# Kernel optimization log

Measured on AMD Instinct MI355X. Metric: run time of the kernel, lower is better.

Reference implementation:

```python
import jax, jax.numpy as jnp
import numpy as np

B, LQ, E, R, H = 4, 64, 512, 32, 768
HOP = 2

def _linear(x, W, b):
    return x @ W + b

def setup_inputs() -> dict:
    key = jax.random.key(0)
    ks = jax.random.split(key, 20)
    s = 0.02
    inp = {
        'question_embedding': jax.random.normal(ks[0], (B, LQ, H), jnp.float32),
        'question_mask': jnp.ones((B, LQ), jnp.float32),
        'entity_embedding': jax.random.normal(ks[1], (B, E, H), jnp.float32),
        'rel_embedding': jax.random.normal(ks[2], (B, E, R, H), jnp.float32),
        'adj': jax.random.randint(ks[3], (B, E, R), 0, E, jnp.int32),
        'node_mask': jax.random.bernoulli(ks[4], 0.95, (B, E)).astype(jnp.float32),
        'adj_mask': jax.random.bernoulli(ks[5], 0.9, (B, E, R)).astype(jnp.float32),
        # params (Linear: y = x @ W + b, W is [in, out])
        'proj_W': jax.random.normal(ks[6], (H, H), jnp.float32) * s,
        'proj_b': jnp.zeros((H,), jnp.float32),
        'rproj_W': jax.random.normal(ks[7], (H, H), jnp.float32) * s,
        'rproj_b': jnp.zeros((H,), jnp.float32),
        'msg_W': jax.random.normal(ks[8], (HOP, 2 * H, H), jnp.float32) * s,
        'msg_b': jnp.zeros((HOP, H), jnp.float32),
        'upd_W': jax.random.normal(ks[9], (HOP, 2 * H, H), jnp.float32) * s,
        'upd_b': jnp.zeros((HOP, H), jnp.float32),
        'relscore_W': jax.random.normal(ks[10], (2 * H, 1), jnp.float32) * s,
        'relscore_b': jnp.zeros((1,), jnp.float32),
        'score_W': jax.random.normal(ks[11], (H, 1), jnp.float32) * s,
        'score_b': jnp.zeros((1,), jnp.float32),
    }
    return inp

def reference(question_embedding, question_mask, entity_embedding, rel_embedding,
              adj, node_mask, adj_mask,
              proj_W, proj_b, rproj_W, rproj_b, msg_W, msg_b, upd_W, upd_b,
              relscore_W, relscore_b, score_W, score_b):
    gelu = lambda x: jax.nn.gelu(x, approximate=False)  # torch nn.GELU default is erf
    dtype = rel_embedding.dtype
    NEG = jnp.finfo(dtype).min

    qe = _linear(question_embedding, proj_W, proj_b)          # [B,LQ,H]
    ee = _linear(entity_embedding, proj_W, proj_b)            # [B,E,H]
    re = _linear(rel_embedding, rproj_W, rproj_b)             # [B,E,R,H]

    qm = question_mask[..., None]
    q = jnp.sum(qe * qm, axis=1) / jnp.sum(qm, axis=1)        # [B,H]

    weight_mask = (1.0 - adj_mask) * NEG                      # [B,E,R]
    q_exp = jnp.broadcast_to(q[:, None, None, :], (B, E, R, H))
    weight_logit = (_linear(jnp.concatenate([re, q_exp], -1), relscore_W, relscore_b)
                    .squeeze(-1) + weight_mask)               # [B,E,R]
    weight = adj_mask * jax.nn.softmax(weight_logit, axis=-1) # [B,E,R]

    adj_flat = adj.reshape(B, E * R)
    for k in range(HOP):
        tail = jnp.take_along_axis(ee, adj_flat[:, :, None], axis=1).reshape(B, E, R, H)
        messages = gelu(_linear(jnp.concatenate([re, tail], -1), msg_W[k], msg_b[k]))
        agg = jnp.einsum('berh,ber->beh', messages, weight)
        ee = gelu(_linear(jnp.concatenate([ee, agg], -1), upd_W[k], upd_b[k]))

    node_neg = (1.0 - node_mask[..., None]) * NEG
    ent_score = (_linear(ee, score_W, score_b) + node_neg).squeeze(-1)  # [B,E]

    # triple_sim (computed under no_grad in torch)
    ee_c = jax.lax.stop_gradient(ee)
    q_c = jax.lax.stop_gradient(q)
    q_source = jnp.einsum('bh,beh->be', q_c, ee_c)            # source node e repeated over R
    q_source = jnp.broadcast_to(q_source[:, :, None], (B, E, R)).reshape(B, E * R)
    tail_final = jnp.take_along_axis(ee_c, adj_flat[:, :, None], axis=1)
    q_target = jnp.einsum('bh,bnh->bn', q_c, tail_final)      # [B,E*R]
    triple_sim = q_source + q_target + jax.lax.stop_gradient(weight_logit).reshape(B, E * R)

    return (ee, ent_score, weight_logit, triple_sim)
```

## Files before the change

### kernel.cpp

```cpp
#include <hip/hip_runtime.h>

#define NEGF (-3.0e38f)

#define BB 4
#define LQQ 64
#define EE_N 512
#define RR 32
#define HH 768

#define WS_QBAR 0
#define WS_Q    3072
#define WS_QD   6144
#define WS_WR1C 6656
#define WS_D0   7424
#define WS_D1   8192
#define WS_C0   8960
#define WS_C1   598784
#define WS_EEA  1188608
#define WS_EEB  2761472
#define WS_EEW  4334336
#define WS_W    5907200
#define WS_AGG  5972736
#define WS_SDOT 7545600
#define WS_CKT0 7547648
#define WS_CKT1 7842560
#define WS_PWT  8137472
#define WS_W0BT 8432384
#define WS_W1BT 8727296
#define WS_U0TT 9022208
#define WS_U0BT 9317120
#define WS_U1TT 9612032
#define WS_U1BT 9906944
#define WS_M0TT 10201856
#define WS_M1TT 10496768
#define WS_RELBF 10791680
#define WS_NEED_BYTES 143830016ull

typedef __attribute__((ext_vector_type(8))) short short8v;
typedef __attribute__((ext_vector_type(4))) short short4v;
typedef __attribute__((ext_vector_type(4))) float f32x4;

#define GLOAD_LDS16(gp, lp) __builtin_amdgcn_global_load_lds( \
    (const __attribute__((address_space(1))) void*)(gp), \
    (__attribute__((address_space(3))) void*)(lp), 16, 0, 0)

__device__ __forceinline__ float gelu_erf(float x) {
    return 0.5f * x * (1.0f + erff(x * 0.70710678118654752f));
}

__device__ __forceinline__ unsigned short f2bf(float f) {
    unsigned int u = __float_as_uint(f);
    unsigned int r = (u + 0x7fffu + ((u >> 16) & 1u)) >> 16;
    return (unsigned short)r;
}

__device__ __forceinline__ float bf2f(unsigned short h) {
    return __uint_as_float(((unsigned int)h) << 16);
}

__global__ void k_qbar(const float* __restrict__ QE, const float* __restrict__ QM,
                       float* __restrict__ qbar) {
    int b = blockIdx.x;
    int tid = threadIdx.x;
    float msum = 0.f;
    for (int l = 0; l < LQQ; ++l) msum += QM[b*LQQ + l];
    for (int h = tid; h < HH; h += 256) {
        float s = 0.f;
        for (int l = 0; l < LQQ; ++l)
            s += QM[b*LQQ + l] * QE[((size_t)(b*LQQ + l))*HH + h];
        qbar[b*HH + h] = s / msum;
    }
}

__global__ void k_small2(const float* __restrict__ RW, const float* __restrict__ RB,
                         const float* __restrict__ RSW, const float* __restrict__ RSB,
                         const float* __restrict__ q, float* __restrict__ wr1c,
                         float* __restrict__ qd) {
    const int wid = threadIdx.x >> 6, lane = threadIdx.x & 63;
    const int blk = blockIdx.x;
    if (blk < 192) {
        int row = blk*4 + wid;
        const float* a = RW + (size_t)row*HH;
        float acc = 0.f;
        #pragma unroll
        for (int p = 0; p < 3; ++p) {
            int i4 = (p*64 + lane) << 2;
            float4 x = *(const float4*)(a + i4);
            float4 w = *(const float4*)(RSW + i4);
            acc += x.x*w.x + x.y*w.y + x.z*w.z + x.w*w.w;
        }
        for (int off = 32; off; off >>= 1) acc += __shfl_xor(acc, off);
        if (lane == 0) wr1c[row] = acc;
    } else {
        float acc = 0.f, acc2 = 0.f;
        const float* src = q + wid*HH;
        #pragma unroll
        for (int p = 0; p < 3; ++p) {
            int i4 = (p*64 + lane) << 2;
            float4 x = *(const float4*)(src + i4);
            float4 w = *(const float4*)(RSW + HH + i4);
            acc += x.x*w.x + x.y*w.y + x.z*w.z + x.w*w.w;
            if (wid == 0) {
                float4 rb = *(const float4*)(RB + i4);
                float4 w0 = *(const float4*)(RSW + i4);
                acc2 += rb.x*w0.x + rb.y*w0.y + rb.z*w0.z + rb.w*w0.w;
            }
        }
        for (int off = 32; off; off >>= 1) { acc += __shfl_xor(acc, off); acc2 += __shfl_xor(acc2, off); }
        if (lane == 0) qd[wid] = acc;
        if (wid == 0 && lane == 0) qd[BB] = acc2 + RSB[0];
    }
}

__global__ void k_dk2(const unsigned short* __restrict__ M0tT,
                      const unsigned short* __restrict__ M1tT,
                      const float* __restrict__ RB, const float* __restrict__ MB,
                      float* __restrict__ d0, float* __restrict__ d1) {
    const int gw = blockIdx.x*4 + (threadIdx.x >> 6);
    const int lane = threadIdx.x & 63;
    const int hop = gw >= HH;
    const int n = hop ? gw - HH : gw;
    const unsigned short* row = (hop ? M1tT : M0tT) + (size_t)n*HH;
    float s = 0.f;
    #pragma unroll
    for (int p = 0; p < 3; ++p) {
        int i4 = (p*64 + lane) << 2;
        const unsigned short* hp = row + i4;
        float4 rv = *(const float4*)(RB + i4);
        s += bf2f(hp[0])*rv.x + bf2f(hp[1])*rv.y + bf2f(hp[2])*rv.z + bf2f(hp[3])*rv.w;
    }
    for (int off = 32; off; off >>= 1) s += __shfl_xor(s, off);
    if (lane == 0) (hop ? d1 : d0)[n] = s + MB[hop*HH + n];
}

__global__ __launch_bounds__(256) void gemm_f32(
    const float* __restrict__ A1, const float* __restrict__ W1,
    const float* __restrict__ bias, float* __restrict__ C,
    int M, int N, int K, int act)
{
    __shared__ float Asm[16][68];
    __shared__ float Bs[16][68];
    const int tid = threadIdx.x;
    const int n0 = blockIdx.x * 64;
    const int m0 = blockIdx.y * 64;
    const int tm = tid >> 4;
    const int tn = tid & 15;
    float acc[4][4] = {};
    for (int kk = 0; kk < K; kk += 16) {
        const int ar = tid >> 2;
        const int ak = (tid & 3) << 2;
        float4 av = make_float4(0.f, 0.f, 0.f, 0.f);
        if (m0 + ar < M) av = *(const float4*)(A1 + (size_t)(m0 + ar)*K + kk + ak);
        const int br = tid >> 4;
        const int bc = (tid & 15) << 2;
        float4 bv = *(const float4*)(W1 + (size_t)(kk + br)*N + n0 + bc);
        __syncthreads();
        Asm[ak+0][ar] = av.x; Asm[ak+1][ar] = av.y;
        Asm[ak+2][ar] = av.z; Asm[ak+3][ar] = av.w;
        *(float4*)&Bs[br][bc] = bv;
        __syncthreads();
        #pragma unroll
        for (int k = 0; k < 16; ++k) {
            float4 a4 = *(const float4*)&Asm[k][tm << 2];
            float4 b4 = *(const float4*)&Bs[k][tn << 2];
            float a[4] = {a4.x, a4.y, a4.z, a4.w};
            float b[4] = {b4.x, b4.y, b4.z, b4.w};
            #pragma unroll
            for (int i = 0; i < 4; ++i)
                #pragma unroll
                for (int j = 0; j < 4; ++j)
                    acc[i][j] = fmaf(a[i], b[j], acc[i][j]);
        }
    }
    float4 bb = make_float4(0.f, 0.f, 0.f, 0.f);
    if (bias) bb = *(const float4*)(bias + n0 + (tn << 2));
    float bbv[4] = {bb.x, bb.y, bb.z, bb.w};
    #pragma unroll
    for (int i = 0; i < 4; ++i) {
        int m = m0 + (tm << 2) + i;
        if (m >= M) break;
        #pragma unroll
        for (int j = 0; j < 4; ++j) {
            float v = acc[i][j] + bbv[j];
            if (act) v = gelu_erf(v);
            C[(size_t)m*N + n0 + (tn << 2) + j] = v;
        }
    }
}

__global__ void k_ckt(const float* __restrict__ Ck, unsigned short* __restrict__ CkT) {
    __shared__ float t[32][33];
    const int k0 = blockIdx.x * 32, n0 = blockIdx.y * 32;
    const int tid = threadIdx.x;
    {
        int r = tid >> 3;
        int c4 = (tid & 7) << 2;
        float4 v = *(const float4*)(Ck + (size_t)(k0 + r)*HH + n0 + c4);
        t[r][c4+0] = v.x; t[r][c4+1] = v.y; t[r][c4+2] = v.z; t[r][c4+3] = v.w;
    }
    __syncthreads();
    {
        int n = tid >> 3;
        int k4 = (tid & 7) << 2;
        unsigned short o[4];
        #pragma unroll
        for (int j = 0; j < 4; ++j) o[j] = f2bf(t[k4+j][n]);
        *(uint2*)(CkT + (size_t)(n0 + n)*HH + k0 + k4) = *(const uint2*)o;
    }
}

struct WPairs { const float* s[9]; unsigned short* d[9]; };
__global__ void k_w2bf(WPairs p) {
    __shared__ float t[32][33];
    const float* __restrict__ Ck = p.s[blockIdx.z];
    unsigned short* __restrict__ CkT = p.d[blockIdx.z];
    const int k0 = blockIdx.x * 32, n0 = blockIdx.y * 32;
    const int tid = threadIdx.x;
    {
        int r = tid >> 3;
        int c4 = (tid & 7) << 2;
        float4 v = *(const float4*)(Ck + (size_t)(k0 + r)*HH + n0 + c4);
        t[r][c4+0] = v.x; t[r][c4+1] = v.y; t[r][c4+2] = v.z; t[r][c4+3] = v.w;
    }
    __syncthreads();
    {
        int n = tid >> 3;
        int k4 = (tid & 7) << 2;
        unsigned short o[4];
        #pragma unroll
        for (int j = 0; j < 4; ++j) o[j] = f2bf(t[k4+j][n]);
        *(uint2*)(CkT + (size_t)(n0 + n)*HH + k0 + k4) = *(const uint2*)o;
    }
}

__global__ __launch_bounds__(256) void k_cvt(
    const float* __restrict__ rel, const float* __restrict__ wr1c,
    const float* __restrict__ qd, const float* __restrict__ am,
    unsigned short* __restrict__ relbf, float* __restrict__ logit) {
    const int wid = threadIdx.x >> 6, lane = threadIdx.x & 63;
    const long row = (long)blockIdx.x*4 + wid;
    const float* a = rel + row*HH;
    unsigned short* o = relbf + row*HH;
    float acc = 0.f;
    #pragma unroll
    for (int p = 0; p < 3; ++p) {
        int i4 = (p*64 + lane) << 2;
        float4 x = *(const float4*)(a + i4);
        float4 wv = *(const float4*)(wr1c + i4);
        acc += x.x*wv.x + x.y*wv.y + x.z*wv.z + x.w*wv.w;
        unsigned short h[4] = {f2bf(x.x), f2bf(x.y), f2bf(x.z), f2bf(x.w)};
        *(uint2*)(o + i4) = *(const uint2*)h;
    }
    for (int off = 32; off; off >>= 1) acc += __shfl_xor(acc, off);
    if (lane == 0) {
        int b = (int)(row >> 14);
        logit[row] = acc + qd[b] + qd[BB] + (1.0f - am[row]) * NEGF;
    }
}

__global__ void k_softmax(const float* __restrict__ logit, const float* __restrict__ am,
                          float* __restrict__ weight) {
    int row = blockIdx.x;
    int lane = threadIdx.x;
    if (lane < 32) {
        float l = logit[row*RR + lane];
        float m = l;
        for (int off = 16; off; off >>= 1) m = fmaxf(m, __shfl_xor(m, off, 32));
        float e = expf(l - m);
        float s = e;
        for (int off = 16; off; off >>= 1) s += __shfl_xor(s, off, 32);
        weight[row*RR + lane] = am[row*RR + lane] * e / s;
    }
}

template<int BM>
__global__ __launch_bounds__(256) void gemm_bf16(
    const float* __restrict__ A1, const unsigned short* __restrict__ W1T,
    const float* __restrict__ A2, const unsigned short* __restrict__ W2T,
    const float* __restrict__ bias, float* __restrict__ C, int act)
{
    constexpr int FM = BM / 32;
    constexpr int AC = BM / 16;
    __shared__ alignas(16) unsigned short As[BM*64];
    __shared__ alignas(16) unsigned short Bs[128*64];
    const int tid = threadIdx.x;
    const int n0 = blockIdx.x * 128;
    const int m0 = blockIdx.y * BM;
    const int w = tid >> 6, lane = tid & 63;
    const int wm = w >> 1, wn = w & 1;
    const int l15 = lane & 15, l4 = lane >> 4;
    const int am_row = tid >> 4;
    const int am_col = (tid & 15) * 4;
    const int bm_row = tid >> 3;
    const int bm_col = (tid & 7) * 8;
    f32x4 acc[FM][4];
    #pragma unroll
    for (int i = 0; i < FM; ++i)
        #pragma unroll
        for (int j = 0; j < 4; ++j) acc[i][j] = (f32x4){0.f,0.f,0.f,0.f};
    const int nPass = (A2 != nullptr) ? 2 : 1;
    for (int pass = 0; pass < nPass; ++pass) {
        const float* __restrict__ A = pass ? A2 : A1;
        const unsigned short* __restrict__ WT = pass ? W2T : W1T;
        for (int k0 = 0; k0 < HH; k0 += 64) {
            float4 av[AC];
            #pragma unroll
            for (int c = 0; c < AC; ++c)
                av[c] = *(const float4*)(A + (size_t)(m0 + c*16 + am_row)*HH + k0 + am_col);
            short8v bv[4];
            #pragma unroll
            for (int i = 0; i < 4; ++i)
                bv[i] = *(const short8v*)(WT + (size_t)(n0 + i*32 + bm_row)*HH + k0 + bm_col);
            __syncthreads();
            #pragma unroll
            for (int c = 0; c < AC; ++c) {
                int r = c*16 + am_row;
                short4v h;
                h[0]=(short)f2bf(av[c].x); h[1]=(short)f2bf(av[c].y);
                h[2]=(short)f2bf(av[c].z); h[3]=(short)f2bf(av[c].w);
                int ba = r*128 + ((am_col*2) ^ ((r & 7) << 4));
                *(short4v*)&As[ba >> 1] = h;
            }
            #pragma unroll
            for (int i = 0; i < 4; ++i) {
                int r = i*32 + bm_row;
                int ba = r*128 + ((bm_col*2) ^ ((r & 7) << 4));
                *(short8v*)&Bs[ba >> 1] = bv[i];
            }
            __syncthreads();
            #pragma unroll
            for (int ks = 0; ks < 2; ++ks) {
                const int kb = ks*64 + l4*16;
                short8v af[FM], bf[4];
                #pragma unroll
                for (int fm = 0; fm < FM; ++fm) {
                    int row = wm*(FM*16) + fm*16 + l15;
                    af[fm] = *(const short8v*)&As[(row*128 + (kb ^ ((row & 7) << 4))) >> 1];
                }
                #pragma unroll
                for (int fn = 0; fn < 4; ++fn) {
                    int row = wn*64 + fn*16 + l15;
                    bf[fn] = *(const short8v*)&Bs[(row*128 + (kb ^ ((row & 7) << 4))) >> 1];
                }
                #pragma unroll
                for (int fm = 0; fm < FM; ++fm)
                    #pragma unroll
                    for (int fn = 0; fn < 4; ++fn)
                        acc[fm][fn] = __builtin_amdgcn_mfma_f32_16x16x32_bf16(af[fm], bf[fn], acc[fm][fn], 0, 0, 0);
            }
            __syncthreads();
        }
    }
    #pragma unroll
    for (int fn = 0; fn < 4; ++fn) {
        int col = n0 + wn*64 + fn*16 + l15;
        float bb = bias ? bias[col] : 0.f;
        #pragma unroll
        for (int fm = 0; fm < FM; ++fm) {
            int row0 = m0 + wm*(FM*16) + fm*16 + l4*4;
            #pragma unroll
            for (int j = 0; j < 4; ++j) {
                float v = acc[fm][fn][j] + bb;
                if (act) v = gelu_erf(v);
                C[(size_t)(row0 + j)*HH + col] = v;
            }
        }
    }
}

__global__ __launch_bounds__(256, 3) void k_msg8(
    const unsigned short* __restrict__ relbf, const unsigned short* __restrict__ CkT,
    const float* __restrict__ dk, const float* __restrict__ eeW,
    const float* __restrict__ weight, const int* __restrict__ adj,
    float* __restrict__ agg)
{
    __shared__ alignas(16) unsigned short As[128*64];
    __shared__ alignas(16) unsigned short Bs[128*64];
    int*   adjS = (int*)As;
    float* wS   = (float*)(As + 256);
    const int tid = threadIdx.x;
    const int bid = blockIdx.x;
    const int L = (bid & 7) * 384 + (bid >> 3);
    const int mt = L / 6, nt = L - mt*6;
    const int n0 = nt * 128;
    const int m0 = mt * 128;
    const int be0 = mt * 4;
    const int b = be0 >> 9;
    const int w = tid >> 6, lane = tid & 63;
    const int wm = w >> 1, wn = w & 1;
    const int l15 = lane & 15, l4 = lane >> 4;
    const int crow = lane >> 3;
    const int csl  = (lane & 7) ^ crow;

    f32x4 acc[4][4];
    #pragma unroll
    for (int i = 0; i < 4; ++i)
        #pragma unroll
        for (int j = 0; j < 4; ++j) acc[i][j] = (f32x4){0.f,0.f,0.f,0.f};

    for (int t = 0; t < 12; ++t) {
        const int k0 = t*64;
        #pragma unroll
        for (int c = 0; c < 4; ++c) {
            int rbase = w*32 + c*8;
            GLOAD_LDS16(relbf + (size_t)(m0 + rbase + crow)*HH + k0 + csl*8,
                        &As[rbase*64]);
            GLOAD_LDS16(CkT   + (size_t)(n0 + rbase + crow)*HH + k0 + csl*8,
                        &Bs[rbase*64]);
        }
        __syncthreads();
        #pragma unroll
        for (int ks = 0; ks < 2; ++ks) {
            const int ko = ks*32 + l4*8;
            short8v af[4], bf[4];
            #pragma unroll
            for (int fm = 0; fm < 4; ++fm) {
                int row = wm*64 + fm*16 + l15;
                af[fm] = *(const short8v*)&As[row*64 + (ko ^ ((row & 7) << 3))];
            }
            #pragma unroll
            for (int fn = 0; fn < 4; ++fn) {
                int row = wn*64 + fn*16 + l15;
                bf[fn] = *(const short8v*)&Bs[row*64 + (ko ^ ((row & 7) << 3))];
            }
            #pragma unroll
            for (int fm = 0; fm < 4; ++fm)
                #pragma unroll
                for (int fn = 0; fn < 4; ++fn)
                    acc[fm][fn] = __builtin_amdgcn_mfma_f32_16x16x32_bf16(af[fm], bf[fn], acc[fm][fn], 0, 0, 0);
        }
        __syncthreads();
    }

    if (tid < 128) {
        adjS[tid] = adj[be0*RR + tid];
        wS[tid]   = weight[be0*RR + tid];
    }
    __syncthreads();

    #pragma unroll
    for (int eh = 0; eh < 2; ++eh) {
        const int el = wm*2 + eh;
        const int be = be0 + el;
        #pragma unroll
        for (int fn = 0; fn < 4; ++fn) {
            int col = n0 + wn*64 + fn*16 + l15;
            float d = dk[col];
            float s = 0.f;
            #pragma unroll
            for (int fp = 0; fp < 2; ++fp) {
                const int fm = eh*2 + fp;
                #pragma unroll
                for (int j = 0; j < 4; ++j) {
                    int rr = fp*16 + l4*4 + j;
                    int tl = adjS[el*RR + rr];
                    float tail = eeW[((size_t)(b*EE_N + tl))*HH + col];
                    s += wS[el*RR + rr] * gelu_erf(acc[fm][fn][j] + tail + d);
                }
            }
            s += __shfl_xor(s, 16);
            s += __shfl_xor(s, 32);
            if (l4 == 0) agg[(size_t)be*HH + col] = s;
        }
    }
}

template<int FUSE>
__global__ __launch_bounds__(256, 3) void k_msg6(
    const float* __restrict__ rel, const unsigned short* __restrict__ CkT,
    const float* __restrict__ dk, const float* __restrict__ eeW,
    const float* __restrict__ weight_in, const int* __restrict__ adj,
    const float* __restrict__ wr1c, const float* __restrict__ qd,
    const float* __restrict__ am,
    float* __restrict__ agg, float* __restrict__ logit_out,
    float* __restrict__ weight_out)
{
    __shared__ alignas(16) unsigned short As[64*64];
    __shared__ alignas(16) unsigned short Bs[256*64];
    int*   adjS = (int*)As;
    float* wS   = (float*)(As + 128);
    float* lgS  = (float*)(As + 256);
    const int tid = threadIdx.x;
    const int bid = blockIdx.x;
    const int L = (bid & 7) * 384 + (bid >> 3);
    const int mt = L / 3, nt = L - mt*3;
    const int n0 = nt * 256;
    const int m0 = mt * 64;
    const int be0 = mt * 2;
    const int b = be0 >> 9;
    const int wn = tid >> 6, lane = tid & 63;
    const int l15 = lane & 15, l4 = lane >> 4;
    const int am_row = tid >> 4;
    const int am_col = (tid & 15) * 4;
    const int bm_row = tid >> 3;
    const int bm_col = (tid & 7) * 8;
    const float* apA = rel + (size_t)(m0 + am_row)*HH + am_col;
    const unsigned short* apB = CkT + (size_t)(n0 + bm_row)*HH + bm_col;
    f32x4 acc[4][4];
    #pragma unroll
    for (int i = 0; i < 4; ++i)
        #pragma unroll
        for (int j = 0; j < 4; ++j) acc[i][j] = (f32x4){0.f,0.f,0.f,0.f};
    float lg[4] = {0.f, 0.f, 0.f, 0.f};
    float4 av[4];
    short8v bv[8];
    #pragma unroll
    for (int c = 0; c < 4; ++c) av[c] = *(const float4*)(apA + (size_t)c*16*HH);
    #pragma unroll
    for (int i = 0; i < 8; ++i) bv[i] = *(const short8v*)(apB + (size_t)i*32*HH);
    for (int t = 0; t < 12; ++t) {
        const int k0 = t*64;
        #pragma unroll
        for (int c = 0; c < 4; ++c) {
            int r = c*16 + am_row;
            short4v h;
            h[0]=(short)f2bf(av[c].x); h[1]=(short)f2bf(av[c].y);
            h[2]=(short)f2bf(av[c].z); h[3]=(short)f2bf(av[c].w);
            int ba = r*128 + ((am_col*2) ^ ((r & 7) << 4));
            *(short4v*)&As[ba >> 1] = h;
        }
        #pragma unroll
        for (int i = 0; i < 8; ++i) {
            int r = i*32 + bm_row;
            int ba = r*128 + ((bm_col*2) ^ ((r & 7) << 4));
            *(short8v*)&Bs[ba >> 1] = bv[i];
        }
        if (FUSE) {
            float4 wv = *(const float4*)(wr1c + k0 + am_col);
            #pragma unroll
            for (int c = 0; c < 4; ++c)
                lg[c] += av[c].x*wv.x + av[c].y*wv.y + av[c].z*wv.z + av[c].w*wv.w;
        }
        if (t < 11) {
            #pragma unroll
            for (int c = 0; c < 4; ++c)
                av[c] = *(const float4*)(apA + (size_t)c*16*HH + k0 + 64);
            #pragma unroll
            for (int i = 0; i < 8; ++i)
                bv[i] = *(const short8v*)(apB + (size_t)i*32*HH + k0 + 64);
        }
        __syncthreads();
        #pragma unroll
        for (int ks = 0; ks < 2; ++ks) {
            const int kb = ks*64 + l4*16;
            short8v af[4], bf[4];
            #pragma unroll
            for (int fm = 0; fm < 4; ++fm) {
                int row = fm*16 + l15;
                af[fm] = *(const short8v*)&As[(row*128 + (kb ^ ((row & 7) << 4))) >> 1];
            }
            #pragma unroll
            for (int fn = 0; fn < 4; ++fn) {
                int row = wn*64 + fn*16 + l15;
                bf[fn] = *(const short8v*)&Bs[(row*128 + (kb ^ ((row & 7) << 4))) >> 1];
            }
            #pragma unroll
            for (int fm = 0; fm < 4; ++fm)
                #pragma unroll
                for (int fn = 0; fn < 4; ++fn)
                    acc[fm][fn] = __builtin_amdgcn_mfma_f32_16x16x32_bf16(af[fm], bf[fn], acc[fm][fn], 0, 0, 0);
        }
        __syncthreads();
    }
    if (tid < 64) adjS[tid] = adj[be0*RR + tid];
    if (!FUSE && tid < 64) wS[tid] = weight_in[be0*RR + tid];
    if (FUSE) {
        #pragma unroll
        for (int c = 0; c < 4; ++c) {
            lg[c] += __shfl_xor(lg[c], 1);
            lg[c] += __shfl_xor(lg[c], 2);
            lg[c] += __shfl_xor(lg[c], 4);
            lg[c] += __shfl_xor(lg[c], 8);
        }
        if ((tid & 15) == 0) {
            #pragma unroll
            for (int c = 0; c < 4; ++c) lgS[c*16 + am_row] = lg[c];
        }
        __syncthreads();
        if (tid < 64) {
            float amv = am[be0*RR + tid];
            float l = lgS[tid] + qd[b] + qd[BB] + (1.0f - amv) * NEGF;
            float mx = l;
            #pragma unroll
            for (int off = 16; off; off >>= 1) mx = fmaxf(mx, __shfl_xor(mx, off, 32));
            float e = expf(l - mx);
            float sm = e;
            #pragma unroll
            for (int off = 16; off; off >>= 1) sm += __shfl_xor(sm, off, 32);
            float wgt = amv * e / sm;
            wS[tid] = wgt;
            if (nt == 0) {
                logit_out[be0*RR + tid] = l;
                weight_out[be0*RR + tid] = wgt;
            }
        }
    }
    __syncthreads();
    #pragma unroll
    for (int eh = 0; eh < 2; ++eh) {
        const int be = be0 + eh;
        #pragma unroll
        for (int fn = 0; fn < 4; ++fn) {
            int col = n0 + wn*64 + fn*16 + l15;
            float d = dk[col];
            float s = 0.f;
            #pragma unroll
            for (int fp = 0; fp < 2; ++fp) {
                const int fm = eh*2 + fp;
                #pragma unroll
                for (int j = 0; j < 4; ++j) {
                    int rr = fp*16 + l4*4 + j;
                    int tl = adjS[eh*RR + rr];
                    float tail = eeW[((size_t)(b*EE_N + tl))*HH + col];
                    s += wS[eh*RR + rr] * gelu_erf(acc[fm][fn][j] + tail + d);
                }
            }
            s += __shfl_xor(s, 16);
            s += __shfl_xor(s, 32);
            if (l4 == 0) agg[(size_t)be*HH + col] = s;
        }
    }
}

__global__ __launch_bounds__(256) void k_score(const float* __restrict__ ee,
                                               const float* __restrict__ SW,
                                               const float* __restrict__ SB,
                                               const float* __restrict__ NM,
                                               const float* __restrict__ q,
                                               float* __restrict__ score,
                                               float* __restrict__ sdot) {
    const int wid = threadIdx.x >> 6, lane = threadIdx.x & 63;
    const int row = blockIdx.x*4 + wid;
    const int b = row >> 9;
    const float* er = ee + (size_t)row*HH;
    const float* qr = q + b*HH;
    float a1 = 0.f, a2 = 0.f;
    #pragma unroll
    for (int p = 0; p < 3; ++p) {
        int i4 = (p*64 + lane) << 2;
        float4 e4 = *(const float4*)(er + i4);
        float4 s4 = *(const float4*)(SW + i4);
        float4 q4 = *(const float4*)(qr + i4);
        a1 += e4.x*s4.x + e4.y*s4.y + e4.z*s4.z + e4.w*s4.w;
        a2 += e4.x*q4.x + e4.y*q4.y + e4.z*q4.z + e4.w*q4.w;
    }
    for (int off = 32; off; off >>= 1) { a1 += __shfl_xor(a1, off); a2 += __shfl_xor(a2, off); }
    if (lane == 0) {
        score[row] = a1 + SB[0] + (1.0f - NM[row]) * NEGF;
        sdot[row] = a2;
    }
}

__global__ void k_triple(const float* __restrict__ sdot, const int* __restrict__ adj,
                         const float* __restrict__ logit, float* __restrict__ tri) {
    int idx = blockIdx.x*256 + threadIdx.x;
    int b = idx >> 14;
    int n = idx & 16383;
    int e = n >> 5;
    int a = adj[idx];
    tri[idx] = sdot[b*EE_N + e] + sdot[b*EE_N + a] + logit[idx];
}

extern "C" void kernel_launch(void* const* d_in, const int* in_sizes, int n_in,
                              void* d_out, int out_size, void* d_ws, size_t ws_size,
                              hipStream_t stream) {
    const float* QE  = (const float*)d_in[0];
    const float* QM  = (const float*)d_in[1];
    const float* ENT = (const float*)d_in[2];
    const float* REL = (const float*)d_in[3];
    const int*   ADJ = (const int*)d_in[4];
    const float* NM  = (const float*)d_in[5];
    const float* AM  = (const float*)d_in[6];
    const float* PW  = (const float*)d_in[7];
    const float* PB  = (const float*)d_in[8];
    const float* RW  = (const float*)d_in[9];
    const float* RB  = (const float*)d_in[10];
    const float* MW  = (const float*)d_in[11];
    const float* MB  = (const float*)d_in[12];
    const float* UW  = (const float*)d_in[13];
    const float* UB  = (const float*)d_in[14];
    const float* RSW = (const float*)d_in[15];
    const float* RSB = (const float*)d_in[16];
    const float* SW  = (const float*)d_in[17];
    const float* SB  = (const float*)d_in[18];

    float* out = (float*)d_out;
    float* ws  = (float*)d_ws;
    float* o_ee    = out;
    float* o_score = out + 1572864;
    float* o_logit = out + 1574912;
    float* o_tri   = out + 1640448;

    unsigned short* CkT0 = (unsigned short*)(ws + WS_CKT0);
    unsigned short* CkT1 = (unsigned short*)(ws + WS_CKT1);
    unsigned short* PWT  = (unsigned short*)(ws + WS_PWT);
    unsigned short* W0bT = (unsigned short*)(ws + WS_W0BT);
    unsigned short* W1bT = (unsigned short*)(ws + WS_W1BT);
    unsigned short* U0tT = (unsigned short*)(ws + WS_U0TT);
    unsigned short* U0bT = (unsigned short*)(ws + WS_U0BT);
    unsigned short* U1tT = (unsigned short*)(ws + WS_U1TT);
    unsigned short* U1bT = (unsigned short*)(ws + WS_U1BT);
    unsigned short* M0tT = (unsigned short*)(ws + WS_M0TT);
    unsigned short* M1tT = (unsigned short*)(ws + WS_M1TT);
    unsigned short* RELBF = (unsigned short*)(ws + WS_RELBF);

    const bool big = ws_size >= WS_NEED_BYTES;

    const size_t HT = (size_t)2*HH*HH;
    const size_t BOT = (size_t)HH*HH;

    k_qbar<<<BB, 256, 0, stream>>>(QE, QM, ws + WS_QBAR);
    gemm_f32<<<dim3(12,1), 256, 0, stream>>>(ws + WS_QBAR, PW, PB, ws + WS_Q, BB, HH, HH, 0);
    k_small2<<<193, 256, 0, stream>>>(RW, RB, RSW, RSB, ws + WS_Q, ws + WS_WR1C, ws + WS_QD);

    WPairs wp;
    wp.s[0] = PW;            wp.d[0] = PWT;
    wp.s[1] = MW + BOT;      wp.d[1] = W0bT;
    wp.s[2] = MW + HT + BOT; wp.d[2] = W1bT;
    wp.s[3] = UW;            wp.d[3] = U0tT;
    wp.s[4] = UW + BOT;      wp.d[4] = U0bT;
    wp.s[5] = UW + HT;       wp.d[5] = U1tT;
    wp.s[6] = UW + HT + BOT; wp.d[6] = U1bT;
    wp.s[7] = MW;            wp.d[7] = M0tT;
    wp.s[8] = MW + HT;       wp.d[8] = M1tT;
    k_w2bf<<<dim3(24,24,9), 256, 0, stream>>>(wp);

    k_dk2<<<384, 256, 0, stream>>>(M0tT, M1tT, RB, MB, ws + WS_D0, ws + WS_D1);

    gemm_bf16<32><<<dim3(6,24), 256, 0, stream>>>(RW, M0tT, nullptr, nullptr, nullptr,
                                                  ws + WS_C0, 0);
    gemm_bf16<32><<<dim3(6,24), 256, 0, stream>>>(RW, M1tT, nullptr, nullptr, nullptr,
                                                  ws + WS_C1, 0);
    k_ckt<<<dim3(24,24), 256, 0, stream>>>(ws + WS_C0, CkT0);
    k_ckt<<<dim3(24,24), 256, 0, stream>>>(ws + WS_C1, CkT1);

    gemm_bf16<32><<<dim3(6,64), 256, 0, stream>>>(ENT, PWT, nullptr, nullptr, PB,
                                                  ws + WS_EEA, 0);

    if (big) {
        k_cvt<<<16384, 256, 0, stream>>>(REL, ws + WS_WR1C, ws + WS_QD, AM,
                                         RELBF, o_logit);
        k_softmax<<<2048, 64, 0, stream>>>(o_logit, AM, ws + WS_W);

        gemm_bf16<32><<<dim3(6,64), 256, 0, stream>>>(ws + WS_EEA, W0bT, nullptr, nullptr, nullptr,
                                                      ws + WS_EEW, 0);
        k_msg8<<<3072, 256, 0, stream>>>(RELBF, CkT0, ws + WS_D0, ws + WS_EEW,
                                         ws + WS_W, ADJ, ws + WS_AGG);
        gemm_bf16<32><<<dim3(6,64), 256, 0, stream>>>(ws + WS_EEA, U0tT, ws + WS_AGG, U0bT, UB,
                                                      ws + WS_EEB, 1);
        gemm_bf16<32><<<dim3(6,64), 256, 0, stream>>>(ws + WS_EEB, W1bT, nullptr, nullptr, nullptr,
                                                      ws + WS_EEW, 0);
        k_msg8<<<3072, 256, 0, stream>>>(RELBF, CkT1, ws + WS_D1, ws + WS_EEW,
                                         ws + WS_W, ADJ, ws + WS_AGG);
        gemm_bf16<32><<<dim3(6,64), 256, 0, stream>>>(ws + WS_EEB, U1tT, ws + WS_AGG, U1bT,
                                                      UB + HH, o_ee, 1);
    } else {
        gemm_bf16<32><<<dim3(6,64), 256, 0, stream>>>(ws + WS_EEA, W0bT, nullptr, nullptr, nullptr,
                                                      ws + WS_EEW, 0);
        k_msg6<1><<<3072, 256, 0, stream>>>(REL, CkT0, ws + WS_D0, ws + WS_EEW,
                                            nullptr, ADJ, ws + WS_WR1C, ws + WS_QD, AM,
                                            ws + WS_AGG, o_logit, ws + WS_W);
        gemm_bf16<32><<<dim3(6,64), 256, 0, stream>>>(ws + WS_EEA, U0tT, ws + WS_AGG, U0bT, UB,
                                                      ws + WS_EEB, 1);
        gemm_bf16<32><<<dim3(6,64), 256, 0, stream>>>(ws + WS_EEB, W1bT, nullptr, nullptr, nullptr,
                                                      ws + WS_EEW, 0);
        k_msg6<0><<<3072, 256, 0, stream>>>(REL, CkT1, ws + WS_D1, ws + WS_EEW,
                                            ws + WS_W, ADJ, ws + WS_WR1C, ws + WS_QD, AM,
                                            ws + WS_AGG, nullptr, nullptr);
        gemm_bf16<32><<<dim3(6,64), 256, 0, stream>>>(ws + WS_EEB, U1tT, ws + WS_AGG, U1bT,
                                                      UB + HH, o_ee, 1);
    }

    k_score<<<512, 256, 0, stream>>>(o_ee, SW, SB, NM, ws + WS_Q, o_score, ws + WS_SDOT);
    k_triple<<<256, 256, 0, stream>>>(ws + WS_SDOT, ADJ, o_logit, o_tri);
}
```

Baseline: 502.1 us.

## Double-buffer A tiles and prepack B fragments for direct register loads in msg kernel

Adds a k_ckp pass that repacks the bf16 CkT weight into per-lane MFMA fragment order. The new k_msg9 loads B operands straight from global memory into registers instead of staging them through LDS. The A tile (relation embeddings) is now double-buffered in LDS, so the load of the next K-tile overlaps the MFMAs on the current one, and one barrier per step is dropped. The cost is two small extra repack kernels, a larger workspace requirement, and more register pressure from holding the B fragments.

```diff
diff --git a/kernel.cpp b/kernel.cpp
--- a/kernel.cpp
+++ b/kernel.cpp
@@ -34,7 +34,9 @@
 #define WS_M0TT 10201856
 #define WS_M1TT 10496768
 #define WS_RELBF 10791680
-#define WS_NEED_BYTES 143830016ull
+#define WS_CKP0  35957504
+#define WS_CKP1  36252416
+#define WS_NEED_BYTES 146189312ull
 
 typedef __attribute__((ext_vector_type(8))) short short8v;
 typedef __attribute__((ext_vector_type(4))) short short4v;
@@ -209,6 +211,23 @@
     }
 }
 
+__global__ void k_ckp(const unsigned short* __restrict__ CkT,
+                      unsigned short* __restrict__ CkP) {
+    const int nt = blockIdx.x / 12, t = blockIdx.x % 12;
+    const int tid = threadIdx.x;
+    #pragma unroll
+    for (int it = 0; it < 4; ++it) {
+        int idx = it*256 + tid;
+        int f = idx >> 6;
+        int l = idx & 63;
+        int ks = f >> 3, fnG = f & 7;
+        int row = nt*128 + fnG*16 + (l & 15);
+        int kc  = t*64 + ks*32 + (l >> 4)*8;
+        uint2 v = *(const uint2*)(CkT + (size_t)row*HH + kc);
+        *(uint2*)(CkP + ((size_t)((nt*24 + t*2 + ks)*8 + fnG)*512 + l*8)) = v;
+    }
+}
+
 struct WPairs { const float* s[9]; unsigned short* d[9]; };
 __global__ void k_w2bf(WPairs p) {
     __shared__ float t[32][33];
@@ -368,16 +387,16 @@
     }
 }
 
-__global__ __launch_bounds__(256, 3) void k_msg8(
-    const unsigned short* __restrict__ relbf, const unsigned short* __restrict__ CkT,
+__global__ __launch_bounds__(256, 3) void k_msg9(
+    const unsigned short* __restrict__ relbf, const unsigned short* __restrict__ CkP,
     const float* __restrict__ dk, const float* __restrict__ eeW,
     const float* __restrict__ weight, const int* __restrict__ adj,
     float* __restrict__ agg)
 {
-    __shared__ alignas(16) unsigned short As[128*64];
-    __shared__ alignas(16) unsigned short Bs[128*64];
-    int*   adjS = (int*)As;
-    float* wS   = (float*)(As + 256);
+    __shared__ alignas(16) unsigned short As0[128*64];
+    __shared__ alignas(16) unsigned short As1[128*64];
+    int*   adjS = (int*)As0;
+    float* wS   = (float*)(As0 + 256);
     const int tid = threadIdx.x;
     const int bid = blockIdx.x;
     const int L = (bid & 7) * 384 + (bid >> 3);
@@ -391,6 +410,7 @@
     const int l15 = lane & 15, l4 = lane >> 4;
     const int crow = lane >> 3;
     const int csl  = (lane & 7) ^ crow;
+    const unsigned short* ckp = CkP + (size_t)nt * 98304 + (size_t)(wn*4)*512 + lane*8;
 
     f32x4 acc[4][4];
     #pragma unroll
@@ -398,39 +418,61 @@
         #pragma unroll
         for (int j = 0; j < 4; ++j) acc[i][j] = (f32x4){0.f,0.f,0.f,0.f};
 
-    for (int t = 0; t < 12; ++t) {
-        const int k0 = t*64;
-        #pragma unroll
-        for (int c = 0; c < 4; ++c) {
-            int rbase = w*32 + c*8;
-            GLOAD_LDS16(relbf + (size_t)(m0 + rbase + crow)*HH + k0 + csl*8,
-                        &As[rbase*64]);
-            GLOAD_LDS16(CkT   + (size_t)(n0 + rbase + crow)*HH + k0 + csl*8,
-                        &Bs[rbase*64]);
-        }
-        __syncthreads();
-        #pragma unroll
-        for (int ks = 0; ks < 2; ++ks) {
-            const int ko = ks*32 + l4*8;
-            short8v af[4], bf[4];
-            #pragma unroll
-            for (int fm = 0; fm < 4; ++fm) {
-                int row = wm*64 + fm*16 + l15;
-                af[fm] = *(const short8v*)&As[row*64 + (ko ^ ((row & 7) << 3))];
-            }
-            #pragma unroll
-            for (int fn = 0; fn < 4; ++fn) {
-                int row = wn*64 + fn*16 + l15;
-                bf[fn] = *(const short8v*)&Bs[row*64 + (ko ^ ((row & 7) << 3))];
-            }
-            #pragma unroll
-            for (int fm = 0; fm < 4; ++fm)
-                #pragma unroll
-                for (int fn = 0; fn < 4; ++fn)
-                    acc[fm][fn] = __builtin_amdgcn_mfma_f32_16x16x32_bf16(af[fm], bf[fn], acc[fm][fn], 0, 0, 0);
-        }
-        __syncthreads();
-    }
+#define MSG9_STAGE(T1, DST) { \
+    const int k0_ = (T1)*64; \
+    _Pragma("unroll") \
+    for (int c = 0; c < 4; ++c) { \
+        int rbase = w*32 + c*8; \
+        GLOAD_LDS16(relbf + (size_t)(m0 + rbase + crow)*HH + k0_ + csl*8, &DST[rbase*64]); \
+    } }
+
+#define MSG9_BLOAD(T0, BF) { \
+    _Pragma("unroll") \
+    for (int ks = 0; ks < 2; ++ks) \
+        _Pragma("unroll") \
+        for (int fn = 0; fn < 4; ++fn) \
+            BF[ks][fn] = *(const short8v*)(ckp + ((size_t)((T0)*2 + ks)*8 + fn)*512); \
+    }
+
+#define MSG9_MATH(SRC, BF) { \
+    _Pragma("unroll") \
+    for (int ks = 0; ks < 2; ++ks) { \
+        const int ko = ks*32 + l4*8; \
+        short8v af[4]; \
+        _Pragma("unroll") \
+        for (int fm = 0; fm < 4; ++fm) { \
+            int row = wm*64 + fm*16 + l15; \
+            af[fm] = *(const short8v*)&SRC[row*64 + (ko ^ ((row & 7) << 3))]; \
+        } \
+        _Pragma("unroll") \
+        for (int fm = 0; fm < 4; ++fm) \
+            _Pragma("unroll") \
+            for (int fn = 0; fn < 4; ++fn) \
+                acc[fm][fn] = __builtin_amdgcn_mfma_f32_16x16x32_bf16(af[fm], BF[ks][fn], acc[fm][fn], 0, 0, 0); \
+    } }
+
+    MSG9_STAGE(0, As0);
+    __syncthreads();
+    for (int tt = 0; tt < 6; ++tt) {
+        const int t0 = tt*2;
+        {
+            short8v bfr[2][4];
+            MSG9_BLOAD(t0, bfr);
+            MSG9_STAGE(t0+1, As1);
+            MSG9_MATH(As0, bfr);
+            __syncthreads();
+        }
+        {
+            short8v bfr[2][4];
+            MSG9_BLOAD(t0+1, bfr);
+            if (tt < 5) MSG9_STAGE(t0+2, As0);
+            MSG9_MATH(As1, bfr);
+            __syncthreads();
+        }
+    }
+#undef MSG9_STAGE
+#undef MSG9_BLOAD
+#undef MSG9_MATH
 
     if (tid < 128) {
         adjS[tid] = adj[be0*RR + tid];
@@ -703,6 +745,8 @@
     unsigned short* M0tT = (unsigned short*)(ws + WS_M0TT);
     unsigned short* M1tT = (unsigned short*)(ws + WS_M1TT);
     unsigned short* RELBF = (unsigned short*)(ws + WS_RELBF);
+    unsigned short* CkP0 = (unsigned short*)(ws + WS_CKP0);
+    unsigned short* CkP1 = (unsigned short*)(ws + WS_CKP1);
 
     const bool big = ws_size >= WS_NEED_BYTES;
 
@@ -733,6 +777,10 @@
                                                   ws + WS_C1, 0);
     k_ckt<<<dim3(24,24), 256, 0, stream>>>(ws + WS_C0, CkT0);
     k_ckt<<<dim3(24,24), 256, 0, stream>>>(ws + WS_C1, CkT1);
+    if (big) {
+        k_ckp<<<72, 256, 0, stream>>>(CkT0, CkP0);
+        k_ckp<<<72, 256, 0, stream>>>(CkT1, CkP1);
+    }
 
     gemm_bf16<32><<<dim3(6,64), 256, 0, stream>>>(ENT, PWT, nullptr, nullptr, PB,
                                                   ws + WS_EEA, 0);
@@ -744,13 +792,13 @@
 
         gemm_bf16<32><<<dim3(6,64), 256, 0, stream>>>(ws + WS_EEA, W0bT, nullptr, nullptr, nullptr,
                                                       ws + WS_EEW, 0);
-        k_msg8<<<3072, 256, 0, stream>>>(RELBF, CkT0, ws + WS_D0, ws + WS_EEW,
+        k_msg9<<<3072, 256, 0, stream>>>(RELBF, CkP0, ws + WS_D0, ws + WS_EEW,
                                          ws + WS_W, ADJ, ws + WS_AGG);
         gemm_bf16<32><<<dim3(6,64), 256, 0, stream>>>(ws + WS_EEA, U0tT, ws + WS_AGG, U0bT, UB,
                                                       ws + WS_EEB, 1);
         gemm_bf16<32><<<dim3(6,64), 256, 0, stream>>>(ws + WS_EEB, W1bT, nullptr, nullptr, nullptr,
                                                       ws + WS_EEW, 0);
-        k_msg8<<<3072, 256, 0, stream>>>(RELBF, CkT1, ws + WS_D1, ws + WS_EEW,
+        k_msg9<<<3072, 256, 0, stream>>>(RELBF, CkP1, ws + WS_D1, ws + WS_EEW,
                                          ws + WS_W, ADJ, ws + WS_AGG);
         gemm_bf16<32><<<dim3(6,64), 256, 0, stream>>>(ws + WS_EEB, U1tT, ws + WS_AGG, U1bT,
                                                       UB + HH, o_ee, 1);
```

New measurement: 579.0 us. 15.3% more time.

## Fuse rel conversion, logit and softmax into first-hop message kernel

Applied to the files above, without the earlier changes.

Adds k_msg10, which reads fp32 rel embeddings directly, converts them to bf16 for the MFMA tile, writes the bf16 copy for the second hop only from nt==0 blocks, and computes the relation logit and masked softmax in-kernel. It replaces the separate k_cvt, k_softmax and k_msg8 launches for hop 0 in the big path. The aim is to drop one full pass over the large rel tensor and two launches. In exchange each of the six N-tile blocks redundantly reads fp32 rel (twice the bytes of bf16) and recomputes the logit dot product, and the conversion adds register pressure inside the GEMM loop.

```diff
diff --git a/kernel.cpp b/kernel.cpp
--- a/kernel.cpp
+++ b/kernel.cpp
@@ -435,6 +435,143 @@
     if (tid < 128) {
         adjS[tid] = adj[be0*RR + tid];
         wS[tid]   = weight[be0*RR + tid];
+    }
+    __syncthreads();
+
+    #pragma unroll
+    for (int eh = 0; eh < 2; ++eh) {
+        const int el = wm*2 + eh;
+        const int be = be0 + el;
+        #pragma unroll
+        for (int fn = 0; fn < 4; ++fn) {
+            int col = n0 + wn*64 + fn*16 + l15;
+            float d = dk[col];
+            float s = 0.f;
+            #pragma unroll
+            for (int fp = 0; fp < 2; ++fp) {
+                const int fm = eh*2 + fp;
+                #pragma unroll
+                for (int j = 0; j < 4; ++j) {
+                    int rr = fp*16 + l4*4 + j;
+                    int tl = adjS[el*RR + rr];
+                    float tail = eeW[((size_t)(b*EE_N + tl))*HH + col];
+                    s += wS[el*RR + rr] * gelu_erf(acc[fm][fn][j] + tail + d);
+                }
+            }
+            s += __shfl_xor(s, 16);
+            s += __shfl_xor(s, 32);
+            if (l4 == 0) agg[(size_t)be*HH + col] = s;
+        }
+    }
+}
+
+__global__ __launch_bounds__(256, 3) void k_msg10(
+    const float* __restrict__ rel, const unsigned short* __restrict__ CkT,
+    const float* __restrict__ dk, const float* __restrict__ eeW,
+    const int* __restrict__ adj, const float* __restrict__ wr1c,
+    const float* __restrict__ qd, const float* __restrict__ am,
+    unsigned short* __restrict__ relbf, float* __restrict__ agg,
+    float* __restrict__ logit_out, float* __restrict__ weight_out)
+{
+    __shared__ alignas(16) unsigned short As[128*64];
+    __shared__ alignas(16) unsigned short Bs[128*64];
+    int*   adjS = (int*)As;
+    float* wS   = (float*)(As + 256);
+    float* lgS  = (float*)(As + 512);
+    const int tid = threadIdx.x;
+    const int bid = blockIdx.x;
+    const int L = (bid & 7) * 384 + (bid >> 3);
+    const int mt = L / 6, nt = L - mt*6;
+    const int n0 = nt * 128;
+    const int m0 = mt * 128;
+    const int be0 = mt * 4;
+    const int b = be0 >> 9;
+    const int w = tid >> 6, lane = tid & 63;
+    const int wm = w >> 1, wn = w & 1;
+    const int l15 = lane & 15, l4 = lane >> 4;
+    const int crow = lane >> 3;
+    const int csl  = (lane & 7) ^ crow;
+    const int arow = tid >> 1, aseg = tid & 1;
+    const float* ap = rel + (size_t)(m0 + arow)*HH + aseg*32;
+    unsigned short* rp = relbf + (size_t)(m0 + arow)*HH + aseg*32;
+
+    f32x4 acc[4][4];
+    #pragma unroll
+    for (int i = 0; i < 4; ++i)
+        #pragma unroll
+        for (int j = 0; j < 4; ++j) acc[i][j] = (f32x4){0.f,0.f,0.f,0.f};
+    float lg = 0.f;
+
+    for (int t = 0; t < 12; ++t) {
+        const int k0 = t*64;
+        #pragma unroll
+        for (int c = 0; c < 4; ++c) {
+            int rbase = w*32 + c*8;
+            GLOAD_LDS16(CkT + (size_t)(n0 + rbase + crow)*HH + k0 + csl*8,
+                        &Bs[rbase*64]);
+        }
+        float4 av[8];
+        #pragma unroll
+        for (int i = 0; i < 8; ++i) av[i] = *(const float4*)(ap + k0 + i*4);
+        #pragma unroll
+        for (int i = 0; i < 4; ++i) {
+            short8v h;
+            float4 x = av[2*i], y = av[2*i+1];
+            h[0]=(short)f2bf(x.x); h[1]=(short)f2bf(x.y); h[2]=(short)f2bf(x.z); h[3]=(short)f2bf(x.w);
+            h[4]=(short)f2bf(y.x); h[5]=(short)f2bf(y.y); h[6]=(short)f2bf(y.z); h[7]=(short)f2bf(y.w);
+            int col = aseg*32 + i*8;
+            *(short8v*)&As[arow*64 + (col ^ ((arow & 7) << 3))] = h;
+            if (nt == 0) *(short8v*)(rp + k0 + i*8) = h;
+        }
+        #pragma unroll
+        for (int i = 0; i < 8; ++i) {
+            float4 wv = *(const float4*)(wr1c + k0 + aseg*32 + i*4);
+            lg += av[i].x*wv.x + av[i].y*wv.y + av[i].z*wv.z + av[i].w*wv.w;
+        }
+        __syncthreads();
+        #pragma unroll
+        for (int ks = 0; ks < 2; ++ks) {
+            const int ko = ks*32 + l4*8;
+            short8v af[4], bf[4];
+            #pragma unroll
+            for (int fm = 0; fm < 4; ++fm) {
+                int row = wm*64 + fm*16 + l15;
+                af[fm] = *(const short8v*)&As[row*64 + (ko ^ ((row & 7) << 3))];
+            }
+            #pragma unroll
+            for (int fn = 0; fn < 4; ++fn) {
+                int row = wn*64 + fn*16 + l15;
+                bf[fn] = *(const short8v*)&Bs[row*64 + (ko ^ ((row & 7) << 3))];
+            }
+            #pragma unroll
+            for (int fm = 0; fm < 4; ++fm)
+                #pragma unroll
+                for (int fn = 0; fn < 4; ++fn)
+                    acc[fm][fn] = __builtin_amdgcn_mfma_f32_16x16x32_bf16(af[fm], bf[fn], acc[fm][fn], 0, 0, 0);
+        }
+        __syncthreads();
+    }
+
+    lg += __shfl_xor(lg, 1);
+    if (aseg == 0) lgS[arow] = lg;
+    if (tid < 128) adjS[tid] = adj[be0*RR + tid];
+    __syncthreads();
+    if (tid < 128) {
+        float amv = am[be0*RR + tid];
+        float l = lgS[tid] + qd[b] + qd[BB] + (1.0f - amv) * NEGF;
+        float mx = l;
+        #pragma unroll
+        for (int off = 16; off; off >>= 1) mx = fmaxf(mx, __shfl_xor(mx, off, 32));
+        float e = expf(l - mx);
+        float sm = e;
+        #pragma unroll
+        for (int off = 16; off; off >>= 1) sm += __shfl_xor(sm, off, 32);
+        float wgt = amv * e / sm;
+        wS[tid] = wgt;
+        if (nt == 0) {
+            logit_out[be0*RR + tid]  = l;
+            weight_out[be0*RR + tid] = wgt;
+        }
     }
     __syncthreads();
 
@@ -738,14 +875,11 @@
                                                   ws + WS_EEA, 0);
 
     if (big) {
-        k_cvt<<<16384, 256, 0, stream>>>(REL, ws + WS_WR1C, ws + WS_QD, AM,
-                                         RELBF, o_logit);
-        k_softmax<<<2048, 64, 0, stream>>>(o_logit, AM, ws + WS_W);
-
         gemm_bf16<32><<<dim3(6,64), 256, 0, stream>>>(ws + WS_EEA, W0bT, nullptr, nullptr, nullptr,
                                                       ws + WS_EEW, 0);
-        k_msg8<<<3072, 256, 0, stream>>>(RELBF, CkT0, ws + WS_D0, ws + WS_EEW,
-                                         ws + WS_W, ADJ, ws + WS_AGG);
+        k_msg10<<<3072, 256, 0, stream>>>(REL, CkT0, ws + WS_D0, ws + WS_EEW,
+                                          ADJ, ws + WS_WR1C, ws + WS_QD, AM,
+                                          RELBF, ws + WS_AGG, o_logit, ws + WS_W);
         gemm_bf16<32><<<dim3(6,64), 256, 0, stream>>>(ws + WS_EEA, U0tT, ws + WS_AGG, U0bT, UB,
                                                       ws + WS_EEB, 1);
         gemm_bf16<32><<<dim3(6,64), 256, 0, stream>>>(ws + WS_EEB, W1bT, nullptr, nullptr, nullptr,
```

Result: slower. 667.9 us (+33.0%).
